# Kernel tuning notes

Hardware: AMD Instinct MI355X
Metric: run time of the kernel (lower is better)

The kernel has to match this reference:

```python
import jax, jax.numpy as jnp
import numpy as np

D_MODEL = 1024
N_HEADS = 16
D_K = D_MODEL // N_HEADS


def _glorot(key, fan_in, fan_out):
    limit = np.sqrt(6.0 / (fan_in + fan_out)).astype(np.float32)
    return jax.random.uniform(key, (fan_in, fan_out), jnp.float32, -limit, limit)


def setup_inputs() -> dict:
    key = jax.random.key(0)
    kx, kq, kk, kv = jax.random.split(key, 4)
    x = jax.random.normal(kx, (2, 2048, D_MODEL), jnp.float32)
    Wq = _glorot(kq, D_MODEL, D_MODEL)
    Wk = _glorot(kk, D_MODEL, D_MODEL)
    Wv = _glorot(kv, D_MODEL, D_MODEL)
    bq = jnp.zeros((D_MODEL,), jnp.float32)
    bk = jnp.zeros((D_MODEL,), jnp.float32)
    bv = jnp.zeros((D_MODEL,), jnp.float32)
    return {"x": x, "Wq": Wq, "bq": bq, "Wk": Wk, "bk": bk, "Wv": Wv, "bv": bv}


def reference(x, Wq, bq, Wk, bk, Wv, bv):
    B, S, _ = x.shape
    # QKV projections (Dense layers with bias)
    q = (x @ Wq + bq).reshape(B, S, N_HEADS, D_K).transpose(0, 2, 1, 3)  # [B,H,S,Dk]
    k = (x @ Wk + bk).reshape(B, S, N_HEADS, D_K).transpose(0, 2, 1, 3)
    v = (x @ Wv + bv).reshape(B, S, N_HEADS, D_K).transpose(0, 2, 1, 3)
    # raw exp-based softmax (NO max subtraction, per original module)
    scores = jnp.einsum('bhqd,bhkd->bhqk', q, k) / np.sqrt(D_K).astype(np.float32)
    scores = jnp.exp(scores)
    attn = scores / (jnp.sum(scores, axis=-1, keepdims=True) + 1e-8)
    context = jnp.einsum('bhqk,bhkd->bhqd', attn, v)  # [B,H,S,Dk]
    return context.transpose(0, 2, 1, 3).reshape(B, S, N_HEADS * D_K)
```

## Files before the change

kernel.cpp:

```cpp
#include <hip/hip_runtime.h>
#include <hip/hip_bf16.h>
#include <stdint.h>

typedef __bf16 bf16x8 __attribute__((ext_vector_type(8)));
typedef __bf16 bf16x4 __attribute__((ext_vector_type(4)));
typedef float  f32x4  __attribute__((ext_vector_type(4)));
typedef short  s16x4  __attribute__((ext_vector_type(4)));
typedef unsigned short u16_t;

#define MFMA(a, b, c)   __builtin_amdgcn_mfma_f32_16x16x32_bf16((a), (b), (c), 0, 0, 0)
#define MFMA16(a, b, c) __builtin_amdgcn_mfma_f32_16x16x16bf16_1k((a), (b), (c), 0, 0, 0)

__device__ __forceinline__ void cp16(const void* g, void* l) {
  __builtin_amdgcn_global_load_lds(
      (const __attribute__((address_space(1))) unsigned int*)g,
      (__attribute__((address_space(3))) unsigned int*)l, 16, 0, 0);
}

__global__ __launch_bounds__(256) void k_prep(const float* __restrict__ x,
                                              const float* __restrict__ W0,
                                              const float* __restrict__ W1,
                                              const float* __restrict__ W2,
                                              u16_t* __restrict__ xb,
                                              u16_t* __restrict__ Wt) {
  __shared__ u16_t T[64][65];
  int bx = blockIdx.x, t = threadIdx.x;
  if (bx < 4096) {
    int i = bx * 256 + t;
    float4 f = ((const float4*)x)[i];
    bf16x4 o = {(__bf16)f.x, (__bf16)f.y, (__bf16)f.z, (__bf16)f.w};
    *(bf16x4*)&xb[(size_t)i * 4] = o;
    return;
  }
  int j = bx - 4096;
  int nx = j & 15, ny = (j >> 4) & 15, z = j >> 8;
  const float* W = z == 0 ? W0 : (z == 1 ? W1 : W2);
  int k0 = ny * 64, n0 = nx * 64;
#pragma unroll
  for (int i = 0; i < 16; i++) {
    int e = i * 256 + t, r = e >> 6, c = e & 63;
    __bf16 hv = (__bf16)W[(size_t)(k0 + r) * 1024 + n0 + c];
    T[r][c] = *(u16_t*)&hv;
  }
  __syncthreads();
  size_t base = ((size_t)z * 1024 + n0) * 1024 + k0;
#pragma unroll
  for (int i = 0; i < 16; i++) {
    int e = i * 256 + t, r = e >> 6, c = e & 63;
    Wt[base + (size_t)r * 1024 + c] = T[c][r];
  }
}

__global__ __launch_bounds__(256, 4) void k_gemm_qkv(
    const u16_t* __restrict__ A, const u16_t* __restrict__ Bt,
    const float* __restrict__ bq, const float* __restrict__ bk,
    const float* __restrict__ bv,
    u16_t* __restrict__ Qo, u16_t* __restrict__ Ko, u16_t* __restrict__ Vo) {
  __shared__ u16_t As[128 * 64];
  __shared__ u16_t Bs[128 * 64];
  const int tid = threadIdx.x, lane = tid & 63, wv = tid >> 6;
  const int quad = lane >> 4, col = lane & 15;
  const int wm = wv >> 1, wn = wv & 1;
  const int tn = blockIdx.x * 128, tm = blockIdx.y * 128;
  f32x4 acc[4][4] = {};

  const int r8 = lane >> 3, c8 = lane & 7;
  const int lch = c8 ^ r8;

  for (int kk = 0; kk < 1024; kk += 64) {
#pragma unroll
    for (int i = 0; i < 4; i++) {
      int blk = wv * 4 + i;
      int m = blk * 8 + r8;
      cp16(A + (size_t)(tm + m) * 1024 + kk + lch * 8, As + blk * 512 + lane * 8);
      cp16(Bt + (size_t)(tn + m) * 1024 + kk + lch * 8, Bs + blk * 512 + lane * 8);
    }
    __syncthreads();
#pragma unroll
    for (int ks = 0; ks < 2; ks++) {
      bf16x8 af[4], bfv[4];
#pragma unroll
      for (int mt = 0; mt < 4; mt++) {
        int row = wm * 64 + mt * 16 + col;
        af[mt] = *(const bf16x8*)&As[row * 64 + (((ks * 4 + quad) ^ (row & 7)) * 8)];
      }
#pragma unroll
      for (int nt = 0; nt < 4; nt++) {
        int row = wn * 64 + nt * 16 + col;
        bfv[nt] = *(const bf16x8*)&Bs[row * 64 + (((ks * 4 + quad) ^ (row & 7)) * 8)];
      }
#pragma unroll
      for (int mt = 0; mt < 4; mt++)
#pragma unroll
        for (int nt = 0; nt < 4; nt++)
          acc[mt][nt] = MFMA(af[mt], bfv[nt], acc[mt][nt]);
    }
    __syncthreads();
  }

  const int mat = tn >> 10;
  const float* bias = mat == 0 ? bq : (mat == 1 ? bk : bv);
  if (mat == 2) {
#pragma unroll
    for (int nt = 0; nt < 4; nt++) {
      int gn = tn + wn * 64 + nt * 16 + col;
      int d = gn & 1023, h = d >> 6, dk = d & 63;
      float bb = bias[d];
#pragma unroll
      for (int mt = 0; mt < 4; mt++) {
        int gm = tm + wm * 64 + mt * 16 + quad * 4;
        int b = gm >> 11, s = gm & 2047;
        bf16x4 pk4;
#pragma unroll
        for (int r = 0; r < 4; r++) pk4[r] = (__bf16)(acc[mt][nt][r] + bb);
        *(bf16x4*)&Vo[((size_t)((b * 16 + h) * 64 + dk)) * 2048 + s] = pk4;
      }
    }
  } else {
    u16_t* O = mat == 0 ? Qo : Ko;
    const float scl = mat == 0 ? 0.18033688011112042f : 1.0f;
#pragma unroll
    for (int nt = 0; nt < 4; nt++) {
      int gn = tn + wn * 64 + nt * 16 + col;
      int d = gn & 1023, h = d >> 6, dk = d & 63;
      float bb = bias[d];
#pragma unroll
      for (int mt = 0; mt < 4; mt++) {
#pragma unroll
        for (int r = 0; r < 4; r++) {
          int gm = tm + wm * 64 + mt * 16 + quad * 4 + r;
          int b = gm >> 11, s = gm & 2047;
          __bf16 hv = (__bf16)((acc[mt][nt][r] + bb) * scl);
          O[((size_t)((b * 16 + h) * 2048 + s)) * 64 + dk] = *(u16_t*)&hv;
        }
      }
    }
  }
}

__global__ __launch_bounds__(256, 4) void k_attn(const u16_t* __restrict__ Q,
                                                 const u16_t* __restrict__ K,
                                                 const u16_t* __restrict__ Vt,
                                                 float* __restrict__ out) {
  __shared__ u16_t smem[20480];
  u16_t* Qs  = smem;
  u16_t* Ksb = smem + 4096;
  u16_t* Vsb = smem + 12288;
  const int tid = threadIdx.x, lane = tid & 63, wv = tid >> 6;
  const int quad = lane >> 4, col = lane & 15;
  const int qh = wv >> 1, kh = wv & 1;

  const int bid = blockIdx.x;
  const int bh = (bid & 7) + 8 * ((bid >> 3) >> 5);
  const int qt = (bid >> 3) & 31;
  const int b = bh >> 4, h = bh & 15;
  const int r8 = lane >> 3, c8 = lane & 7;

  const u16_t* Qg = Q + ((size_t)bh * 2048 + qt * 64) * 64;
  const u16_t* Kg = K + (size_t)bh * 2048 * 64;
  const u16_t* Vg = Vt + (size_t)bh * 64 * 2048;

#pragma unroll
  for (int i = 0; i < 2; i++) {
    int c = wv * 2 + i;
    int row = c * 8 + r8;
    int lch = c8 ^ r8;
    cp16(Qg + (size_t)row * 64 + lch * 8, Qs + c * 512 + lane * 8);
    cp16(Kg + (size_t)row * 64 + lch * 8, Ksb + c * 512 + lane * 8);
    cp16(Vg + (size_t)row * 2048 + lch * 8, Vsb + c * 512 + lane * 8);
  }
  __syncthreads();

  bf16x8 qf[2][2];
#pragma unroll
  for (int nt = 0; nt < 2; nt++)
#pragma unroll
    for (int ks = 0; ks < 2; ks++) {
      int row = qh * 32 + nt * 16 + col;
      qf[nt][ks] = *(const bf16x8*)&Qs[row * 64 + (((ks * 4 + quad) ^ (row & 7)) * 8)];
    }

  const short one_bf = (short)0x3F80;
  s16x4 ones4 = {one_bf, one_bf, one_bf, one_bf};

  f32x4 ao[2][4] = {};
  f32x4 dn[2] = {};

#pragma unroll 2
  for (int kt = 0; kt < 32; kt++) {
    const int cur = kt & 1;
    const u16_t* Kc = Ksb + cur * 4096;
    const u16_t* Vc = Vsb + cur * 4096;
    if (kt + 1 < 32) {
      u16_t* Kn = Ksb + (cur ^ 1) * 4096;
      u16_t* Vn = Vsb + (cur ^ 1) * 4096;
#pragma unroll
      for (int i = 0; i < 2; i++) {
        int c = wv * 2 + i;
        int row = c * 8 + r8;
        int lch = c8 ^ r8;
        cp16(Kg + (size_t)(kt + 1) * 4096 + (size_t)row * 64 + lch * 8,
             Kn + c * 512 + lane * 8);
        cp16(Vg + (size_t)row * 2048 + (kt + 1) * 64 + lch * 8,
             Vn + c * 512 + lane * 8);
      }
    }

    f32x4 sc[2][2] = {};
#pragma unroll
    for (int ks = 0; ks < 2; ks++) {
      bf16x8 kf[2];
#pragma unroll
      for (int mt = 0; mt < 2; mt++) {
        int row = kh * 32 + mt * 16 + col;
        kf[mt] = *(const bf16x8*)&Kc[row * 64 + (((ks * 4 + quad) ^ (row & 7)) * 8)];
      }
#pragma unroll
      for (int mt = 0; mt < 2; mt++)
#pragma unroll
        for (int nt = 0; nt < 2; nt++)
          sc[mt][nt] = MFMA(kf[mt], qf[nt][ks], sc[mt][nt]);
    }

    s16x4 pf[2][2];
#pragma unroll
    for (int mt = 0; mt < 2; mt++)
#pragma unroll
      for (int nt = 0; nt < 2; nt++) {
#pragma unroll
        for (int r = 0; r < 4; r++) {
          __bf16 e = (__bf16)__builtin_amdgcn_exp2f(sc[mt][nt][r]);
          pf[mt][nt][r] = *(short*)&e;
        }
        dn[nt] = MFMA16(pf[mt][nt], ones4, dn[nt]);
      }

#pragma unroll
    for (int mt = 0; mt < 2; mt++) {
#pragma unroll
      for (int dt = 0; dt < 4; dt++) {
        int row = dt * 16 + col;
        int c = kh * 4 + mt * 2 + (quad >> 1);
        int addr = row * 64 + ((c ^ (row & 7)) * 8) + (quad & 1) * 4;
        s16x4 vf = *(const s16x4*)&Vc[addr];
#pragma unroll
        for (int nt = 0; nt < 2; nt++)
          ao[nt][dt] = MFMA16(pf[mt][nt], vf, ao[nt][dt]);
      }
    }
    __syncthreads();
  }

  float* red = (float*)(smem + 4096);
  const int rb = (qh * 64 + lane) * 41;
  if (kh == 1) {
#pragma unroll
    for (int nt = 0; nt < 2; nt++) {
#pragma unroll
      for (int dt = 0; dt < 4; dt++)
#pragma unroll
        for (int r = 0; r < 4; r++)
          red[rb + (nt * 4 + dt) * 4 + r] = ao[nt][dt][r];
#pragma unroll
      for (int r = 0; r < 4; r++)
        red[rb + 32 + nt * 4 + r] = dn[nt][r];
    }
  }
  __syncthreads();
  if (kh == 0) {
#pragma unroll
    for (int nt = 0; nt < 2; nt++) {
      float dsum[4];
#pragma unroll
      for (int r = 0; r < 4; r++)
        dsum[r] = dn[nt][r] + red[rb + 32 + nt * 4 + r] + 1e-8f;
#pragma unroll
      for (int dt = 0; dt < 4; dt++) {
#pragma unroll
        for (int r = 0; r < 4; r++) {
          float v = (ao[nt][dt][r] + red[rb + (nt * 4 + dt) * 4 + r]) / dsum[r];
          int s = qt * 64 + qh * 32 + nt * 16 + quad * 4 + r;
          out[((size_t)b * 2048 + s) * 1024 + h * 64 + dt * 16 + col] = v;
        }
      }
    }
  }
}

extern "C" void kernel_launch(void* const* d_in, const int* in_sizes, int n_in,
                              void* d_out, int out_size, void* d_ws, size_t ws_size,
                              hipStream_t stream) {
  const float* x  = (const float*)d_in[0];
  const float* Wq = (const float*)d_in[1];
  const float* bq = (const float*)d_in[2];
  const float* Wk = (const float*)d_in[3];
  const float* bk = (const float*)d_in[4];
  const float* Wv = (const float*)d_in[5];
  const float* bv = (const float*)d_in[6];
  float* out = (float*)d_out;

  char* ws = (char*)d_ws;
  u16_t* xb  = (u16_t*)(ws);
  u16_t* Wt  = (u16_t*)(ws + 8388608);
  u16_t* Qb  = (u16_t*)(ws + 14680064);
  u16_t* Kb  = (u16_t*)(ws + 23068672);
  u16_t* Vtb = (u16_t*)(ws + 31457280);

  hipLaunchKernelGGL(k_prep, dim3(4864), dim3(256), 0, stream, x, Wq, Wk, Wv, xb, Wt);
  hipLaunchKernelGGL(k_gemm_qkv, dim3(24, 32), dim3(256), 0, stream,
                     xb, Wt, bq, bk, bv, Qb, Kb, Vtb);
  hipLaunchKernelGGL(k_attn, dim3(1024), dim3(256), 0, stream, Qb, Kb, Vtb, out);
}
```

Before: 167.7 us.

## Rewrite QKV GEMM with 256x256 tiles and double-buffered LDS pipeline

Rebuilds the QKV projection GEMM around 256x256 output tiles computed by 512-thread blocks (8 waves). Global-to-LDS copies for the next k-tile are double-buffered and overlapped with MFMA work using explicit barriers, waitcnts and priority hints. Blocks are remapped so that neighbouring blocks share A and B tiles in cache. The aim is to cut load latency and raise data reuse per LDS byte. The costs are 128 KB of shared memory per block, larger accumulator register use, and only 192 blocks, which risks underfilling the 256 CUs.

```diff
diff --git a/kernel.cpp b/kernel.cpp
--- a/kernel.cpp
+++ b/kernel.cpp
@@ -51,52 +51,116 @@
   }
 }
 
-__global__ __launch_bounds__(256, 4) void k_gemm_qkv(
+__global__ __launch_bounds__(512, 2) void k_gemm_qkv(
     const u16_t* __restrict__ A, const u16_t* __restrict__ Bt,
     const float* __restrict__ bq, const float* __restrict__ bk,
     const float* __restrict__ bv,
     u16_t* __restrict__ Qo, u16_t* __restrict__ Ko, u16_t* __restrict__ Vo) {
-  __shared__ u16_t As[128 * 64];
-  __shared__ u16_t Bs[128 * 64];
+  __shared__ u16_t smem[65536];
+  u16_t* As = smem;
+  u16_t* Bs = smem + 32768;
+
   const int tid = threadIdx.x, lane = tid & 63, wv = tid >> 6;
   const int quad = lane >> 4, col = lane & 15;
-  const int wm = wv >> 1, wn = wv & 1;
-  const int tn = blockIdx.x * 128, tm = blockIdx.y * 128;
-  f32x4 acc[4][4] = {};
-
-  const int r8 = lane >> 3, c8 = lane & 7;
-  const int lch = c8 ^ r8;
-
-  for (int kk = 0; kk < 1024; kk += 64) {
-#pragma unroll
-    for (int i = 0; i < 4; i++) {
-      int blk = wv * 4 + i;
-      int m = blk * 8 + r8;
-      cp16(A + (size_t)(tm + m) * 1024 + kk + lch * 8, As + blk * 512 + lane * 8);
-      cp16(Bt + (size_t)(tn + m) * 1024 + kk + lch * 8, Bs + blk * 512 + lane * 8);
-    }
-    __syncthreads();
-#pragma unroll
-    for (int ks = 0; ks < 2; ks++) {
-      bf16x8 af[4], bfv[4];
-#pragma unroll
-      for (int mt = 0; mt < 4; mt++) {
-        int row = wm * 64 + mt * 16 + col;
-        af[mt] = *(const bf16x8*)&As[row * 64 + (((ks * 4 + quad) ^ (row & 7)) * 8)];
-      }
-#pragma unroll
-      for (int nt = 0; nt < 4; nt++) {
-        int row = wn * 64 + nt * 16 + col;
-        bfv[nt] = *(const bf16x8*)&Bs[row * 64 + (((ks * 4 + quad) ^ (row & 7)) * 8)];
-      }
-#pragma unroll
-      for (int mt = 0; mt < 4; mt++)
-#pragma unroll
-        for (int nt = 0; nt < 4; nt++)
-          acc[mt][nt] = MFMA(af[mt], bfv[nt], acc[mt][nt]);
-    }
-    __syncthreads();
-  }
+  const int wm = wv >> 2, wn = wv & 3;
+
+  int bid = blockIdx.x;
+  int wg = (bid & 7) * 24 + (bid >> 3);
+  const int tn = (wg % 12) << 8, tm = (wg / 12) << 8;
+
+  const int r16 = lane >> 2, c4 = lane & 3;
+  const int srow = wv * 16 + r16;
+  const int skoff = ((c4 ^ (r16 & 3)) << 3);
+  const int sdst = srow * 32 + (c4 << 3);
+  const size_t gA0 = (size_t)(tm + srow) * 1024 + skoff;
+  const size_t gB0 = (size_t)(tn + srow) * 1024 + skoff;
+
+  f32x4 acc[8][4] = {};
+
+#define STAGE(kt, h, b) do {                                   \
+    int d_ = (b) * 16384 + (h) * 8192 + sdst;                  \
+    size_t s_ = (size_t)(kt) * 64 + (h) * 32;                  \
+    cp16(A + gA0 + s_, As + d_);                               \
+    cp16(A + gA0 + s_ + (size_t)128 * 1024, As + d_ + 4096);   \
+    cp16(Bt + gB0 + s_, Bs + d_);                              \
+    cp16(Bt + gB0 + s_ + (size_t)128 * 1024, Bs + d_ + 4096);  \
+  } while (0)
+
+#define BAR()    asm volatile("s_barrier" ::: "memory")
+#define WAITV(N) asm volatile("s_waitcnt vmcnt(" #N ")" ::: "memory")
+#define WAITL()  asm volatile("s_waitcnt lgkmcnt(0)" ::: "memory")
+#define SCHED0() __builtin_amdgcn_sched_barrier(0)
+
+  STAGE(0, 0, 0);
+  STAGE(0, 1, 0);
+  WAITV(4);
+  BAR();
+
+  const int swz8 = (((lane >> 4) ^ (col & 3)) << 3);
+  const int abase = (wm * 128 + col) * 32 + swz8;
+  const int bbase = (wn * 64 + col) * 32 + swz8;
+
+  for (int t = 0; t < 16; ++t) {
+    const int cur = t & 1, nxt = cur ^ 1;
+    const u16_t* Ap = As + cur * 16384;
+    const u16_t* Bp = Bs + cur * 16384;
+    bf16x8 af[4], bf[4];
+
+#pragma unroll
+    for (int i = 0; i < 4; i++) af[i] = *(const bf16x8*)&Ap[abase + i * 512];
+#pragma unroll
+    for (int i = 0; i < 4; i++) bf[i] = *(const bf16x8*)&Bp[bbase + i * 512];
+    if (t + 1 < 16) STAGE(t + 1, 0, nxt);
+    BAR(); WAITL(); SCHED0();
+    __builtin_amdgcn_s_setprio(1);
+#pragma unroll
+    for (int i = 0; i < 4; i++)
+#pragma unroll
+      for (int j = 0; j < 4; j++) acc[i][j] = MFMA(af[i], bf[j], acc[i][j]);
+    __builtin_amdgcn_s_setprio(0);
+    BAR();
+
+#pragma unroll
+    for (int i = 0; i < 4; i++) af[i] = *(const bf16x8*)&Ap[abase + (i + 4) * 512];
+    if (t + 1 < 16) { STAGE(t + 1, 1, nxt); WAITV(8); }
+    else            { WAITV(0); }
+    BAR(); WAITL(); SCHED0();
+    __builtin_amdgcn_s_setprio(1);
+#pragma unroll
+    for (int i = 0; i < 4; i++)
+#pragma unroll
+      for (int j = 0; j < 4; j++) acc[i + 4][j] = MFMA(af[i], bf[j], acc[i + 4][j]);
+    __builtin_amdgcn_s_setprio(0);
+    BAR();
+
+#pragma unroll
+    for (int i = 0; i < 4; i++) af[i] = *(const bf16x8*)&Ap[8192 + abase + i * 512];
+#pragma unroll
+    for (int i = 0; i < 4; i++) bf[i] = *(const bf16x8*)&Bp[8192 + bbase + i * 512];
+    BAR(); WAITL(); SCHED0();
+    __builtin_amdgcn_s_setprio(1);
+#pragma unroll
+    for (int i = 0; i < 4; i++)
+#pragma unroll
+      for (int j = 0; j < 4; j++) acc[i][j] = MFMA(af[i], bf[j], acc[i][j]);
+    __builtin_amdgcn_s_setprio(0);
+    BAR();
+
+#pragma unroll
+    for (int i = 0; i < 4; i++) af[i] = *(const bf16x8*)&Ap[8192 + abase + (i + 4) * 512];
+    if (t + 1 < 16) WAITV(4);
+    WAITL();
+    BAR(); SCHED0();
+    __builtin_amdgcn_s_setprio(1);
+#pragma unroll
+    for (int i = 0; i < 4; i++)
+#pragma unroll
+      for (int j = 0; j < 4; j++) acc[i + 4][j] = MFMA(af[i], bf[j], acc[i + 4][j]);
+    __builtin_amdgcn_s_setprio(0);
+    BAR();
+  }
+
+#undef STAGE
 
   const int mat = tn >> 10;
   const float* bias = mat == 0 ? bq : (mat == 1 ? bk : bv);
@@ -107,8 +171,8 @@
       int d = gn & 1023, h = d >> 6, dk = d & 63;
       float bb = bias[d];
 #pragma unroll
-      for (int mt = 0; mt < 4; mt++) {
-        int gm = tm + wm * 64 + mt * 16 + quad * 4;
+      for (int mt = 0; mt < 8; mt++) {
+        int gm = tm + wm * 128 + mt * 16 + quad * 4;
         int b = gm >> 11, s = gm & 2047;
         bf16x4 pk4;
 #pragma unroll
@@ -125,10 +189,10 @@
       int d = gn & 1023, h = d >> 6, dk = d & 63;
       float bb = bias[d];
 #pragma unroll
-      for (int mt = 0; mt < 4; mt++) {
+      for (int mt = 0; mt < 8; mt++) {
 #pragma unroll
         for (int r = 0; r < 4; r++) {
-          int gm = tm + wm * 64 + mt * 16 + quad * 4 + r;
+          int gm = tm + wm * 128 + mt * 16 + quad * 4 + r;
           int b = gm >> 11, s = gm & 2047;
           __bf16 hv = (__bf16)((acc[mt][nt][r] + bb) * scl);
           O[((size_t)((b * 16 + h) * 2048 + s)) * 64 + dk] = *(u16_t*)&hv;
@@ -307,7 +371,7 @@
   u16_t* Vtb = (u16_t*)(ws + 31457280);
 
   hipLaunchKernelGGL(k_prep, dim3(4864), dim3(256), 0, stream, x, Wq, Wk, Wv, xb, Wt);
-  hipLaunchKernelGGL(k_gemm_qkv, dim3(24, 32), dim3(256), 0, stream,
+  hipLaunchKernelGGL(k_gemm_qkv, dim3(192), dim3(512), 0, stream,
                      xb, Wt, bq, bk, bv, Qb, Kb, Vtb);
   hipLaunchKernelGGL(k_attn, dim3(1024), dim3(256), 0, stream, Qb, Kb, Vtb, out);
 }
```

After: 174.7 us. +4.2%, slower.
